# Kernel optimization log

Hardware: AMD Instinct MI355X
Metric: run time of the kernel (lower is better)

Reference implementation:

```python
import jax, jax.numpy as jnp
import numpy as np

# Production-scale dims: tokens T = B*S = 1024, d_model = 768, 8 experts, top-2 routing
B, S, D, E, K = 1, 1024, 768, 8, 2
H = 4 * D  # expert hidden dim


def setup_inputs() -> dict:
    key = jax.random.key(0)
    ks = jax.random.split(key, 6)
    s = jnp.float32(0.02)
    return {
        "x": jax.random.normal(ks[0], (B, S, D), jnp.float32),
        "Wr": jax.random.normal(ks[1], (E, D), jnp.float32) * s,      # router Linear (no bias), torch layout [out,in]
        "W1": jax.random.normal(ks[2], (E, H, D), jnp.float32) * s,   # per-expert first Linear
        "b1": jnp.zeros((E, H), jnp.float32),
        "W2": jax.random.normal(ks[3], (E, D, H), jnp.float32) * s,   # per-expert second Linear
        "b2": jnp.zeros((E, D), jnp.float32),
        "sW1": jax.random.normal(ks[4], (H, D), jnp.float32) * s,     # shared expert
        "sb1": jnp.zeros((H,), jnp.float32),
        "sW2": jax.random.normal(ks[5], (D, H), jnp.float32) * s,
        "sb2": jnp.zeros((D,), jnp.float32),
    }


def reference(x, Wr, W1, b1, W2, b2, sW1, sb1, sW2, sb2):
    Bx, Sx, Dx = x.shape
    xf = x.reshape(-1, Dx)                                   # [T, D]
    T = xf.shape[0]

    # Router: top-k logits, others masked to -inf, then softmax.
    # softmax over -inf-masked logits == softmax over the k kept logits scattered back.
    logits = xf @ Wr.T                                       # [T, E]
    topv, idx = jax.lax.top_k(logits, K)                     # [T, K]
    gate_k = jax.nn.softmax(topv, axis=-1)                   # [T, K]
    gates = jnp.zeros((T, logits.shape[-1]), x.dtype).at[
        jnp.arange(T)[:, None], idx
    ].add(gate_k)                                            # [T, E], zero for unrouted experts

    # Expert MLPs (dense over experts; gate is exactly zero for unrouted -> same math
    # as the original masked gather/scatter loop). Dropout is identity in eval mode.
    h = jax.nn.relu(jnp.einsum('td,ehd->teh', xf, W1) + b1)  # [T, E, H]
    y = jnp.einsum('teh,edh->ted', h, W2) + b2               # [T, E, D]
    moe = jnp.einsum('te,ted->td', gates, y)                 # [T, D]

    # Shared expert: original adds 0.1 * shared(x) once per expert that selected the
    # token; every token is selected by exactly K (distinct top-k) experts.
    sh = jax.nn.relu(xf @ sW1.T + sb1) @ sW2.T + sb2         # [T, D]
    out = moe + (0.1 * K) * sh
    return out.reshape(Bx, Sx, Dx)
```

## Files before the change

### kernel.cpp

```cpp
#include <hip/hip_runtime.h>

#define T_TOK 1024
#define Dm 768
#define Hm 3072
#define NE 8
#define NPACK 3072
#define MAXTILES 32

typedef __attribute__((ext_vector_type(8))) short short8;
typedef __attribute__((ext_vector_type(4))) float f32x4;

__device__ __forceinline__ unsigned f2bf(float f) {
  unsigned u = __builtin_bit_cast(unsigned, f);
  u += 0x7fffu + ((u >> 16) & 1u);
  return u >> 16;
}
__device__ __forceinline__ unsigned pk2bf(float a, float b) {
  return f2bf(a) | (f2bf(b) << 16);
}

__global__ __launch_bounds__(256) void router_kernel(
    const float* __restrict__ x, const float* __restrict__ Wr,
    int* __restrict__ counts, int* __restrict__ tlist, float* __restrict__ glist) {
  __shared__ float sWr[NE * Dm];
  for (int i = threadIdx.x; i < NE * Dm; i += 256) sWr[i] = Wr[i];
  __syncthreads();
  const int wave = threadIdx.x >> 6, lane = threadIdx.x & 63;
  const int t = blockIdx.x * 4 + wave;
  float acc[NE];
#pragma unroll
  for (int e = 0; e < NE; e++) acc[e] = 0.f;
  for (int d = lane; d < Dm; d += 64) {
    float xv = x[t * Dm + d];
#pragma unroll
    for (int e = 0; e < NE; e++) acc[e] += xv * sWr[e * Dm + d];
  }
#pragma unroll
  for (int e = 0; e < NE; e++) {
#pragma unroll
    for (int off = 32; off > 0; off >>= 1) acc[e] += __shfl_down(acc[e], off);
  }
  if (lane == 0) {
    int i0 = 0; float v0 = acc[0];
#pragma unroll
    for (int e = 1; e < NE; e++) if (acc[e] > v0) { v0 = acc[e]; i0 = e; }
    int i1 = -1; float v1 = -1e30f;
#pragma unroll
    for (int e = 0; e < NE; e++) if (e != i0 && acc[e] > v1) { v1 = acc[e]; i1 = e; }
    float g0 = 1.f / (1.f + expf(v1 - v0));
    float g1 = 1.f - g0;
    int p0 = atomicAdd(&counts[i0], 1);
    tlist[i0 * T_TOK + p0] = t; glist[i0 * T_TOK + p0] = g0;
    int p1 = atomicAdd(&counts[i1], 1);
    tlist[i1 * T_TOK + p1] = t; glist[i1 * T_TOK + p1] = g1;
  }
}

__global__ void prefix_kernel(const int* __restrict__ counts, int* __restrict__ bases,
                              int* __restrict__ ntiles, int2* __restrict__ tiles) {
  if (threadIdx.x == 0) {
    int s = 0;
    for (int e = 0; e < NE; e++) { bases[e] = s; s += counts[e]; }
    bases[NE] = s;
    int nt = 0;
    for (int e = 0; e <= NE; e++) {
      int Ne = (e < NE) ? counts[e] : T_TOK;
      for (int m0 = 0; m0 < Ne && nt < MAXTILES; m0 += 128) tiles[nt++] = make_int2(e, m0);
    }
    *ntiles = nt;
  }
}

template <int MODE>
__global__ __launch_bounds__(512) void moe_gemm(
    const float* __restrict__ x,
    const float* __restrict__ W1, const float* __restrict__ b1,
    const float* __restrict__ sW1, const float* __restrict__ sb1,
    const float* __restrict__ W2, const float* __restrict__ b2,
    const float* __restrict__ sW2, const float* __restrict__ sb2,
    unsigned short* __restrict__ hbuf, float* __restrict__ outp,
    const int* __restrict__ counts, const int* __restrict__ bases,
    const int* __restrict__ ntiles, const int2* __restrict__ tiles,
    const int* __restrict__ tlist, const float* __restrict__ glist) {
  const int ti = blockIdx.y;
  if (ti >= *ntiles) return;
  const int2 tl = tiles[ti];
  const int e = tl.x, m0 = tl.y;
  const int Ne = (e < NE) ? counts[e] : T_TOK;
  const int pbase = bases[e];
  const int n0 = blockIdx.x * 128;

  constexpr int Kfull = (MODE == 0) ? Dm : Hm;
  constexpr int KC    = (MODE == 0) ? Dm : (Hm / 2);
  constexpr int NK    = KC / 64;
  const int kbase = (MODE == 0) ? 0 : (blockIdx.z * KC);

  const float* Bw;
  const float* bias;
  if constexpr (MODE == 0) {
    Bw   = (e < NE) ? W1 + (size_t)e * Hm * Dm : sW1;
    bias = (e < NE) ? b1 + (size_t)e * Hm : sb1;
  } else {
    Bw   = (e < NE) ? W2 + (size_t)e * Dm * Hm : sW2;
    bias = (e < NE) ? b2 + (size_t)e * Dm : sb2;
  }

  __shared__ unsigned short sA[128][72];
  __shared__ unsigned short sB[128][72];

  const int tid = threadIdx.x;
  const int lane = tid & 63;
  const int wid = tid >> 6;
  const int wr = wid >> 2;
  const int wc = wid & 3;

  const float* aPtrF[4];
  const unsigned short* aPtrH[2];
  if constexpr (MODE == 0) {
#pragma unroll
    for (int c = 0; c < 4; c++) {
      int gi = m0 + c * 32 + (tid >> 4);
      int si = gi < Ne ? gi : Ne - 1;
      int tok = (e < NE) ? tlist[e * T_TOK + si] : si;
      aPtrF[c] = x + (size_t)tok * Dm + (tid & 15) * 4;
    }
  } else {
#pragma unroll
    for (int c = 0; c < 2; c++) {
      int prow = pbase + m0 + c * 64 + (tid >> 3);
      if (prow >= NPACK) prow = NPACK - 1;
      aPtrH[c] = hbuf + (size_t)prow * Hm + kbase + (tid & 7) * 8;
    }
  }
  const float* bPtrF[4];
#pragma unroll
  for (int c = 0; c < 4; c++) {
    int nrow = n0 + c * 32 + (tid >> 4);
    bPtrF[c] = Bw + (size_t)nrow * Kfull + kbase + (tid & 15) * 4;
  }

  f32x4 acc[4][2];
#pragma unroll
  for (int m = 0; m < 4; m++)
#pragma unroll
    for (int n = 0; n < 2; n++) acc[m][n] = (f32x4)0.0f;

  const int rF = tid >> 4;
  const int cF = (tid & 15) * 4;
  const int rH = tid >> 3;
  const int cH = (tid & 7) * 8;
  const int frow = lane & 15;
  const int fk = (lane >> 4) * 8;

  float4 aF[4], bF[4];
  uint4 aH[2];

  if constexpr (MODE == 0) {
#pragma unroll
    for (int c = 0; c < 4; c++) aF[c] = *(const float4*)(aPtrF[c]);
  } else {
#pragma unroll
    for (int c = 0; c < 2; c++) aH[c] = *(const uint4*)(aPtrH[c]);
  }
#pragma unroll
  for (int c = 0; c < 4; c++) bF[c] = *(const float4*)(bPtrF[c]);

  for (int ks = 0; ks < NK; ks++) {
    if constexpr (MODE == 0) {
#pragma unroll
      for (int c = 0; c < 4; c++) {
        *(uint2*)&sA[c * 32 + rF][cF] =
            make_uint2(pk2bf(aF[c].x, aF[c].y), pk2bf(aF[c].z, aF[c].w));
      }
    } else {
#pragma unroll
      for (int c = 0; c < 2; c++) *(uint4*)&sA[c * 64 + rH][cH] = aH[c];
    }
#pragma unroll
    for (int c = 0; c < 4; c++) {
      *(uint2*)&sB[c * 32 + rF][cF] =
          make_uint2(pk2bf(bF[c].x, bF[c].y), pk2bf(bF[c].z, bF[c].w));
    }
    __syncthreads();

    if (ks + 1 < NK) {
      int ko = (ks + 1) * 64;
      if constexpr (MODE == 0) {
#pragma unroll
        for (int c = 0; c < 4; c++) aF[c] = *(const float4*)(aPtrF[c] + ko);
      } else {
#pragma unroll
        for (int c = 0; c < 2; c++) aH[c] = *(const uint4*)(aPtrH[c] + ko);
      }
#pragma unroll
      for (int c = 0; c < 4; c++) bF[c] = *(const float4*)(bPtrF[c] + ko);
    }

#pragma unroll
    for (int kk = 0; kk < 2; kk++) {
      short8 af[4], bfr[2];
#pragma unroll
      for (int m = 0; m < 4; m++)
        af[m] = *(const short8*)&sA[wr * 64 + m * 16 + frow][kk * 32 + fk];
#pragma unroll
      for (int n = 0; n < 2; n++)
        bfr[n] = *(const short8*)&sB[wc * 32 + n * 16 + frow][kk * 32 + fk];
#pragma unroll
      for (int m = 0; m < 4; m++)
#pragma unroll
        for (int n = 0; n < 2; n++)
          acc[m][n] = __builtin_amdgcn_mfma_f32_16x16x32_bf16(af[m], bfr[n], acc[m][n], 0, 0, 0);
    }
    __syncthreads();
  }

#pragma unroll
  for (int m = 0; m < 4; m++) {
    int lr = wr * 64 + m * 16 + (lane >> 4) * 4;
#pragma unroll
    for (int n = 0; n < 2; n++) {
      int gc = n0 + wc * 32 + n * 16 + (lane & 15);
      float bv = bias[gc];
#pragma unroll
      for (int j = 0; j < 4; j++) {
        int gi = m0 + lr + j;
        if (gi >= Ne) continue;
        float v = acc[m][n][j];
        if constexpr (MODE == 0) {
          v += bv;
          v = v > 0.f ? v : 0.f;
          hbuf[(size_t)(pbase + gi) * Hm + gc] = (unsigned short)f2bf(v);
        } else {
          int t; float g;
          if (e < NE) { t = tlist[e * T_TOK + gi]; g = glist[e * T_TOK + gi]; }
          else        { t = gi; g = 0.2f; }
          float add = g * (v + (kbase == 0 ? bv : 0.f));
          atomicAdd(&outp[(size_t)t * Dm + gc], add);
        }
      }
    }
  }
}

extern "C" void kernel_launch(void* const* d_in, const int* in_sizes, int n_in,
                              void* d_out, int out_size, void* d_ws, size_t ws_size,
                              hipStream_t stream) {
  const float* x   = (const float*)d_in[0];
  const float* Wr  = (const float*)d_in[1];
  const float* W1  = (const float*)d_in[2];
  const float* b1  = (const float*)d_in[3];
  const float* W2  = (const float*)d_in[4];
  const float* b2  = (const float*)d_in[5];
  const float* sW1 = (const float*)d_in[6];
  const float* sb1 = (const float*)d_in[7];
  const float* sW2 = (const float*)d_in[8];
  const float* sb2 = (const float*)d_in[9];
  float* out = (float*)d_out;

  char* ws = (char*)d_ws;
  int*    counts  = (int*)(ws + 0);
  int*    bases   = (int*)(ws + 128);
  int*    ntiles  = (int*)(ws + 192);
  int2*   tiles   = (int2*)(ws + 256);
  int*    tlist   = (int*)(ws + 768);
  float*  glist   = (float*)(ws + 33536);
  unsigned short* hbuf = (unsigned short*)(ws + 66304);

  (void)hipMemsetAsync(counts, 0, 128, stream);
  (void)hipMemsetAsync(out, 0, (size_t)T_TOK * Dm * sizeof(float), stream);

  router_kernel<<<dim3(T_TOK / 4), 256, 0, stream>>>(x, Wr, counts, tlist, glist);
  prefix_kernel<<<1, 64, 0, stream>>>(counts, bases, ntiles, tiles);

  moe_gemm<0><<<dim3(Hm / 128, MAXTILES, 1), 512, 0, stream>>>(
      x, W1, b1, sW1, sb1, W2, b2, sW2, sb2, hbuf, out,
      counts, bases, ntiles, tiles, tlist, glist);
  moe_gemm<1><<<dim3(Dm / 128, MAXTILES, 2), 512, 0, stream>>>(
      x, W1, b1, sW1, sb1, W2, b2, sW2, sb2, hbuf, out,
      counts, bases, ntiles, tiles, tlist, glist);
}
```

Measured before the change: 369.2 us.

## Replace atomic scatter with split-K buffer and gather finalize, drop prefix kernel

Removes the single-thread prefix kernel: each GEMM block now derives its expert tile from counts with an inline scan. The second GEMM writes split-K partials to a workspace buffer instead of atomically adding into the output. A new finalize kernel gathers each token's two expert rows plus the shared row, applying gates and biases, which also removes the output memset. The K loop is restructured into a two-register-stage ping-pong prefetch. The trade is extra global traffic for the partial buffer, one more launch, and a fallback to the atomic path when the workspace is too small.

```diff
diff --git a/kernel.cpp b/kernel.cpp
--- a/kernel.cpp
+++ b/kernel.cpp
@@ -21,7 +21,8 @@
 
 __global__ __launch_bounds__(256) void router_kernel(
     const float* __restrict__ x, const float* __restrict__ Wr,
-    int* __restrict__ counts, int* __restrict__ tlist, float* __restrict__ glist) {
+    int* __restrict__ counts, int* __restrict__ tlist, float* __restrict__ glist,
+    int4* __restrict__ tok2row, float2* __restrict__ tok2g) {
   __shared__ float sWr[NE * Dm];
   for (int i = threadIdx.x; i < NE * Dm; i += 256) sWr[i] = Wr[i];
   __syncthreads();
@@ -53,21 +54,8 @@
     tlist[i0 * T_TOK + p0] = t; glist[i0 * T_TOK + p0] = g0;
     int p1 = atomicAdd(&counts[i1], 1);
     tlist[i1 * T_TOK + p1] = t; glist[i1 * T_TOK + p1] = g1;
-  }
-}
-
-__global__ void prefix_kernel(const int* __restrict__ counts, int* __restrict__ bases,
-                              int* __restrict__ ntiles, int2* __restrict__ tiles) {
-  if (threadIdx.x == 0) {
-    int s = 0;
-    for (int e = 0; e < NE; e++) { bases[e] = s; s += counts[e]; }
-    bases[NE] = s;
-    int nt = 0;
-    for (int e = 0; e <= NE; e++) {
-      int Ne = (e < NE) ? counts[e] : T_TOK;
-      for (int m0 = 0; m0 < Ne && nt < MAXTILES; m0 += 128) tiles[nt++] = make_int2(e, m0);
-    }
-    *ntiles = nt;
+    tok2row[t] = make_int4(i0, p0, i1, p1);
+    tok2g[t] = float2{g0, g1};
   }
 }
 
@@ -78,16 +66,21 @@
     const float* __restrict__ sW1, const float* __restrict__ sb1,
     const float* __restrict__ W2, const float* __restrict__ b2,
     const float* __restrict__ sW2, const float* __restrict__ sb2,
-    unsigned short* __restrict__ hbuf, float* __restrict__ outp,
-    const int* __restrict__ counts, const int* __restrict__ bases,
-    const int* __restrict__ ntiles, const int2* __restrict__ tiles,
+    unsigned short* __restrict__ hbuf, float* __restrict__ ybuf, float* __restrict__ outp,
+    const int* __restrict__ counts,
     const int* __restrict__ tlist, const float* __restrict__ glist) {
-  const int ti = blockIdx.y;
-  if (ti >= *ntiles) return;
-  const int2 tl = tiles[ti];
-  const int e = tl.x, m0 = tl.y;
-  const int Ne = (e < NE) ? counts[e] : T_TOK;
-  const int pbase = bases[e];
+  int ti = blockIdx.y;
+  int e = 0, m0 = 0, pbase = 0, Ne = 0;
+  bool found = false;
+  for (int ee = 0; ee <= NE; ee++) {
+    int ne = (ee < NE) ? counts[ee] : T_TOK;
+    int nt = (ne + 127) >> 7;
+    if (!found) {
+      if (ti < nt) { e = ee; Ne = ne; m0 = ti << 7; found = true; }
+      else { ti -= nt; pbase += ne; }
+    }
+  }
+  if (!found) return;
   const int n0 = blockIdx.x * 128;
 
   constexpr int Kfull = (MODE == 0) ? Dm : Hm;
@@ -152,50 +145,62 @@
   const int frow = lane & 15;
   const int fk = (lane >> 4) * 8;
 
-  float4 aF[4], bF[4];
-  uint4 aH[2];
-
-  if constexpr (MODE == 0) {
-#pragma unroll
-    for (int c = 0; c < 4; c++) aF[c] = *(const float4*)(aPtrF[c]);
-  } else {
-#pragma unroll
-    for (int c = 0; c < 2; c++) aH[c] = *(const uint4*)(aPtrH[c]);
-  }
-#pragma unroll
-  for (int c = 0; c < 4; c++) bF[c] = *(const float4*)(bPtrF[c]);
-
-  for (int ks = 0; ks < NK; ks++) {
+  float4 aFA[4], bFA[4], aFB[4], bFB[4];
+  uint4 aHA[2], aHB[2];
+
+  auto stage_load_A = [&](int ko) {
     if constexpr (MODE == 0) {
 #pragma unroll
-      for (int c = 0; c < 4; c++) {
+      for (int c = 0; c < 4; c++) aFA[c] = *(const float4*)(aPtrF[c] + ko);
+    } else {
+#pragma unroll
+      for (int c = 0; c < 2; c++) aHA[c] = *(const uint4*)(aPtrH[c] + ko);
+    }
+#pragma unroll
+    for (int c = 0; c < 4; c++) bFA[c] = *(const float4*)(bPtrF[c] + ko);
+  };
+  auto stage_load_B = [&](int ko) {
+    if constexpr (MODE == 0) {
+#pragma unroll
+      for (int c = 0; c < 4; c++) aFB[c] = *(const float4*)(aPtrF[c] + ko);
+    } else {
+#pragma unroll
+      for (int c = 0; c < 2; c++) aHB[c] = *(const uint4*)(aPtrH[c] + ko);
+    }
+#pragma unroll
+    for (int c = 0; c < 4; c++) bFB[c] = *(const float4*)(bPtrF[c] + ko);
+  };
+  auto stage_write_A = [&]() {
+    if constexpr (MODE == 0) {
+#pragma unroll
+      for (int c = 0; c < 4; c++)
         *(uint2*)&sA[c * 32 + rF][cF] =
-            make_uint2(pk2bf(aF[c].x, aF[c].y), pk2bf(aF[c].z, aF[c].w));
-      }
+            make_uint2(pk2bf(aFA[c].x, aFA[c].y), pk2bf(aFA[c].z, aFA[c].w));
     } else {
 #pragma unroll
-      for (int c = 0; c < 2; c++) *(uint4*)&sA[c * 64 + rH][cH] = aH[c];
-    }
-#pragma unroll
-    for (int c = 0; c < 4; c++) {
+      for (int c = 0; c < 2; c++) *(uint4*)&sA[c * 64 + rH][cH] = aHA[c];
+    }
+#pragma unroll
+    for (int c = 0; c < 4; c++)
       *(uint2*)&sB[c * 32 + rF][cF] =
-          make_uint2(pk2bf(bF[c].x, bF[c].y), pk2bf(bF[c].z, bF[c].w));
-    }
-    __syncthreads();
-
-    if (ks + 1 < NK) {
-      int ko = (ks + 1) * 64;
-      if constexpr (MODE == 0) {
-#pragma unroll
-        for (int c = 0; c < 4; c++) aF[c] = *(const float4*)(aPtrF[c] + ko);
-      } else {
-#pragma unroll
-        for (int c = 0; c < 2; c++) aH[c] = *(const uint4*)(aPtrH[c] + ko);
-      }
-#pragma unroll
-      for (int c = 0; c < 4; c++) bF[c] = *(const float4*)(bPtrF[c] + ko);
-    }
-
+          make_uint2(pk2bf(bFA[c].x, bFA[c].y), pk2bf(bFA[c].z, bFA[c].w));
+  };
+  auto stage_write_B = [&]() {
+    if constexpr (MODE == 0) {
+#pragma unroll
+      for (int c = 0; c < 4; c++)
+        *(uint2*)&sA[c * 32 + rF][cF] =
+            make_uint2(pk2bf(aFB[c].x, aFB[c].y), pk2bf(aFB[c].z, aFB[c].w));
+    } else {
+#pragma unroll
+      for (int c = 0; c < 2; c++) *(uint4*)&sA[c * 64 + rH][cH] = aHB[c];
+    }
+#pragma unroll
+    for (int c = 0; c < 4; c++)
+      *(uint2*)&sB[c * 32 + rF][cF] =
+          make_uint2(pk2bf(bFB[c].x, bFB[c].y), pk2bf(bFB[c].z, bFB[c].w));
+  };
+  auto do_mfma = [&]() {
 #pragma unroll
     for (int kk = 0; kk < 2; kk++) {
       short8 af[4], bfr[2];
@@ -211,6 +216,21 @@
         for (int n = 0; n < 2; n++)
           acc[m][n] = __builtin_amdgcn_mfma_f32_16x16x32_bf16(af[m], bfr[n], acc[m][n], 0, 0, 0);
     }
+  };
+
+  stage_load_A(0);
+  stage_load_B(64);
+
+  for (int ks = 0; ks < NK; ks += 2) {
+    stage_write_A();
+    __syncthreads();
+    if (ks + 2 < NK) stage_load_A((ks + 2) * 64);
+    do_mfma();
+    __syncthreads();
+    stage_write_B();
+    __syncthreads();
+    if (ks + 3 < NK) stage_load_B((ks + 3) * 64);
+    do_mfma();
     __syncthreads();
   }
 
@@ -230,6 +250,8 @@
           v += bv;
           v = v > 0.f ? v : 0.f;
           hbuf[(size_t)(pbase + gi) * Hm + gc] = (unsigned short)f2bf(v);
+        } else if constexpr (MODE == 1) {
+          ybuf[(size_t)blockIdx.z * NPACK * Dm + (size_t)(pbase + gi) * Dm + gc] = v;
         } else {
           int t; float g;
           if (e < NE) { t = tlist[e * T_TOK + gi]; g = glist[e * T_TOK + gi]; }
@@ -239,6 +261,31 @@
         }
       }
     }
+  }
+}
+
+__global__ __launch_bounds__(256) void finalize_kernel(
+    const float* __restrict__ ybuf, const int* __restrict__ counts,
+    const int4* __restrict__ tok2row, const float2* __restrict__ tok2g,
+    const float* __restrict__ b2, const float* __restrict__ sb2,
+    float* __restrict__ out) {
+  const int t = blockIdx.x;
+  int bases[NE];
+  int s = 0;
+#pragma unroll
+  for (int e = 0; e < NE; e++) { bases[e] = s; s += counts[e]; }
+  const int4 rr = tok2row[t];
+  const float2 gg = tok2g[t];
+  const int r0 = bases[rr.x] + rr.y;
+  const int r1 = bases[rr.z] + rr.w;
+  const int rs = s + t;
+  const float* y0 = ybuf;
+  const float* y1 = ybuf + (size_t)NPACK * Dm;
+  for (int d = threadIdx.x; d < Dm; d += 256) {
+    float v0 = y0[(size_t)r0 * Dm + d] + y1[(size_t)r0 * Dm + d] + b2[rr.x * Dm + d];
+    float v1 = y0[(size_t)r1 * Dm + d] + y1[(size_t)r1 * Dm + d] + b2[rr.z * Dm + d];
+    float vs = y0[(size_t)rs * Dm + d] + y1[(size_t)rs * Dm + d] + sb2[d];
+    out[(size_t)t * Dm + d] = gg.x * v0 + gg.y * v1 + 0.2f * vs;
   }
 }
 
@@ -259,23 +306,30 @@
 
   char* ws = (char*)d_ws;
   int*    counts  = (int*)(ws + 0);
-  int*    bases   = (int*)(ws + 128);
-  int*    ntiles  = (int*)(ws + 192);
-  int2*   tiles   = (int2*)(ws + 256);
-  int*    tlist   = (int*)(ws + 768);
-  float*  glist   = (float*)(ws + 33536);
-  unsigned short* hbuf = (unsigned short*)(ws + 66304);
+  int4*   tok2row = (int4*)(ws + 1024);
+  float2* tok2g   = (float2*)(ws + 17408);
+  int*    tlist   = (int*)(ws + 25600);
+  float*  glist   = (float*)(ws + 58368);
+  unsigned short* hbuf = (unsigned short*)(ws + 91136);
+  float*  ybuf    = (float*)(ws + 18965504);
+  const size_t NEED_YBUF = 37839872;
 
   (void)hipMemsetAsync(counts, 0, 128, stream);
-  (void)hipMemsetAsync(out, 0, (size_t)T_TOK * Dm * sizeof(float), stream);
-
-  router_kernel<<<dim3(T_TOK / 4), 256, 0, stream>>>(x, Wr, counts, tlist, glist);
-  prefix_kernel<<<1, 64, 0, stream>>>(counts, bases, ntiles, tiles);
+
+  router_kernel<<<dim3(T_TOK / 4), 256, 0, stream>>>(x, Wr, counts, tlist, glist,
+                                                     tok2row, tok2g);
 
   moe_gemm<0><<<dim3(Hm / 128, MAXTILES, 1), 512, 0, stream>>>(
-      x, W1, b1, sW1, sb1, W2, b2, sW2, sb2, hbuf, out,
-      counts, bases, ntiles, tiles, tlist, glist);
-  moe_gemm<1><<<dim3(Dm / 128, MAXTILES, 2), 512, 0, stream>>>(
-      x, W1, b1, sW1, sb1, W2, b2, sW2, sb2, hbuf, out,
-      counts, bases, ntiles, tiles, tlist, glist);
-}
+      x, W1, b1, sW1, sb1, W2, b2, sW2, sb2, hbuf, ybuf, out, counts, tlist, glist);
+
+  if (ws_size >= NEED_YBUF) {
+    moe_gemm<1><<<dim3(Dm / 128, MAXTILES, 2), 512, 0, stream>>>(
+        x, W1, b1, sW1, sb1, W2, b2, sW2, sb2, hbuf, ybuf, out, counts, tlist, glist);
+    finalize_kernel<<<dim3(T_TOK), 256, 0, stream>>>(ybuf, counts, tok2row, tok2g,
+                                                     b2, sb2, out);
+  } else {
+    (void)hipMemsetAsync(out, 0, (size_t)T_TOK * Dm * sizeof(float), stream);
+    moe_gemm<2><<<dim3(Dm / 128, MAXTILES, 2), 512, 0, stream>>>(
+        x, W1, b1, sW1, sb1, W2, b2, sW2, sb2, hbuf, ybuf, out, counts, tlist, glist);
+  }
+}
```

After: 371.9 us. About the same (+0.7%).
